# Kernel tuning notes

Measured on AMD Instinct MI355X. Metric: run time of the kernel, lower is better.

Reference implementation:

```python
import math
import jax, jax.numpy as jnp
import numpy as np

HEAD = 8
D_HEAD = 32
D_MODEL = 256
N = 20000
E_LOCAL = 80000
E_BOND = 60000
E_GLOBAL = 400000
MAX_DEG = 32
MAX_DIST = 64


def segment_softmax(x, seg, num_segments):
    # softmax over entries sharing the same segment id (scatter_softmax)
    m = jax.ops.segment_max(x, seg, num_segments=num_segments)
    e = jnp.exp(x - m[seg])
    s = jax.ops.segment_sum(e, seg, num_segments=num_segments)
    return e / s[seg]


def setup_inputs() -> dict:
    key = jax.random.key(0)
    ks = jax.random.split(key, 16)
    s_in = 1.0 / math.sqrt(D_MODEL)
    s_out = 1.0 / math.sqrt(2 * D_MODEL)
    dist_emb = jax.random.normal(ks[7], (MAX_DIST + 1, D_MODEL), jnp.float32) * 0.02
    dist_emb = dist_emb.at[MAX_DIST].set(0.0)  # padding_idx
    return {
        "f_node": jax.random.normal(ks[0], (N, D_MODEL), jnp.float32),
        "f_bond": jax.random.normal(ks[1], (E_BOND, D_MODEL), jnp.float32),
        "deg_matrix": jax.random.randint(ks[2], (N,), 0, MAX_DEG + 1),
        "dist_matrix": jax.random.randint(ks[3], (E_GLOBAL,), 0, MAX_DIST + 1),
        "bond_idx": jax.random.randint(ks[4], (2, E_LOCAL), 0, N),
        "query_idx": jax.random.randint(ks[5], (E_GLOBAL,), 0, N),
        "key_idx": jax.random.randint(ks[6], (E_GLOBAL,), 0, N),
        "attention_bond_idx": jnp.arange(E_BOND),
        "deg_emb": jax.random.normal(ks[8], (MAX_DEG + 1, D_MODEL), jnp.float32) * 0.02,
        "dist_emb": dist_emb,
        "Wq_w": jax.random.normal(ks[9], (D_MODEL, 2 * D_MODEL), jnp.float32) * s_in,
        "Wq_b": jnp.zeros((2 * D_MODEL,), jnp.float32),
        "Wk_w": jax.random.normal(ks[10], (D_MODEL, 2 * D_MODEL), jnp.float32) * s_in,
        "Wk_b": jnp.zeros((2 * D_MODEL,), jnp.float32),
        "Wv_w": jax.random.normal(ks[11], (D_MODEL, 2 * D_MODEL), jnp.float32) * s_in,
        "Wv_b": jnp.zeros((2 * D_MODEL,), jnp.float32),
        "out_w": jax.random.normal(ks[12], (2 * D_MODEL, D_MODEL), jnp.float32) * s_out,
        "out_b": jnp.zeros((D_MODEL,), jnp.float32),
        "bond_emb_w": jax.random.normal(ks[13], (D_MODEL, 2 * D_MODEL), jnp.float32) * s_in,
        "bond_emb_b": jnp.zeros((2 * D_MODEL,), jnp.float32),
        "bond_update_w": jax.random.normal(ks[14], (2 * D_MODEL, D_MODEL), jnp.float32) * s_out,
        "bond_update_b": jnp.zeros((D_MODEL,), jnp.float32),
    }


def reference(f_node, f_bond, deg_matrix, dist_matrix, bond_idx, query_idx, key_idx,
              attention_bond_idx, deg_emb, dist_emb, Wq_w, Wq_b, Wk_w, Wk_b, Wv_w, Wv_b,
              out_w, out_b, bond_emb_w, bond_emb_b, bond_update_w, bond_update_b):
    scale = 1.0 / math.sqrt(D_HEAD)
    n = f_node.shape[0]
    e_bond = f_bond.shape[0]

    f_deg = deg_emb[deg_matrix].reshape(n, HEAD, D_HEAD)                  # [N,H,Dh]
    ab_vb = f_bond @ bond_emb_w + bond_emb_b                               # [Eb,2D]
    attention_bond, value_bond = jnp.split(ab_vb, 2, axis=-1)
    attention_bond = attention_bond.reshape(e_bond, HEAD, D_HEAD)
    value_bond = value_bond.reshape(e_bond, HEAD, D_HEAD)
    f_dist = dist_emb[dist_matrix].reshape(-1, HEAD, D_HEAD)               # [Eg,H,Dh]

    q = (f_node @ Wq_w + Wq_b).reshape(n, 2 * HEAD, D_HEAD)
    k = (f_node @ Wk_w + Wk_b).reshape(n, 2 * HEAD, D_HEAD)
    v = (f_node @ Wv_w + Wv_b).reshape(n, 2 * HEAD, D_HEAD)
    q_local, q_global = q[:, :HEAD], q[:, HEAD:]
    k_local, k_global = k[:, :HEAD], k[:, HEAD:]
    v_local, v_global = v[:, :HEAD], v[:, HEAD:]

    src, dst = bond_idx[0], bond_idx[1]
    # ---- local (bond) attention ----
    score_local = q_local[dst] * k_local[src]                              # [El,H,Dh]
    score_local = score_local.at[:e_bond].add(attention_bond)
    score_local = score_local.sum(-1) * scale                              # [El,H]
    score_local = segment_softmax(score_local, dst, n)
    local_out = v_local[src].at[:e_bond].add(value_bond)
    local_out = local_out * score_local[:, :, None]
    local_out = jax.ops.segment_sum(local_out, dst, num_segments=n)
    local_out = local_out.reshape(n, HEAD * D_HEAD)

    # ---- global (distance) attention ----
    kg = k_global + f_deg
    score_global = q_global[query_idx] * kg[key_idx]                       # [Eg,H,Dh]
    score_global = score_global.at[attention_bond_idx].add(attention_bond)
    score_global = (score_global + f_dist).sum(-1) * scale                 # [Eg,H]
    score_global = segment_softmax(score_global, query_idx, n)
    global_out = v_global[key_idx] * score_global[:, :, None]
    global_out = jax.ops.segment_sum(global_out, query_idx, num_segments=n)
    global_out = global_out.reshape(n, HEAD * D_HEAD)

    out = jnp.concatenate([local_out, global_out], axis=-1) @ out_w + out_b  # [N,D]
    bond_out = jnp.concatenate([f_bond, out[src[:e_bond]]], axis=-1)
    bond_out = bond_out @ bond_update_w + bond_update_b                      # [Eb,D]
    return out, bond_out
```

## Files before the change

### kernel.cpp

```cpp
#include <hip/hip_runtime.h>
#include <math.h>

typedef unsigned short u16;
typedef unsigned int u32;
typedef __attribute__((ext_vector_type(8))) short s16x8;
typedef __attribute__((ext_vector_type(4))) unsigned short u16x4;
typedef __attribute__((ext_vector_type(4))) float f32x4;

__device__ __forceinline__ float bf2f(u16 x) { return __uint_as_float(((u32)x) << 16); }
__device__ __forceinline__ u16 f2bf(float f) {
    u32 u = __float_as_uint(f);
    u32 r = u + 0x7fffu + ((u >> 16) & 1u);
    return (u16)(r >> 16);
}

__device__ __forceinline__ void gll16(const u16* g, u16* l) {
    __builtin_amdgcn_global_load_lds((const __attribute__((address_space(1))) void*)g,
                                     (__attribute__((address_space(3))) void*)l,
                                     16, 0, 0);
}

template <int MODE>
__global__ __launch_bounds__(256) void gemm128(
    const u16* __restrict__ Abf, const u16* __restrict__ A2b,
    const u16* __restrict__ BT, const float* __restrict__ bias,
    u16* __restrict__ Cb, float* __restrict__ Cf, u16* __restrict__ C2b,
    const float* __restrict__ auxemb, const int* __restrict__ auxidx,
    float* __restrict__ absum, int M, int N, int K)
{
    __shared__ u16 lsmem[3 * 8192];

    const int tid = threadIdx.x;
    const int wave = tid >> 6;
    const int lane = tid & 63;
    const int l15 = lane & 15;
    const int quad = lane >> 4;
    const int wr = wave >> 1, wc = wave & 1;
    const int tileRow = blockIdx.y * 128;
    const int tileCol = blockIdx.x * 128;

    const int srow = tid >> 2;
    const int sk8 = (((tid & 3) ^ ((tid >> 3) & 3)) * 8);
    const int r0 = tileRow + srow, r1 = r0 + 64;

    const u16 *gA0, *gA1, *gA0b = nullptr, *gA1b = nullptr;
    if (MODE == 3) {
        gA0 = Abf + (size_t)r0 * 256 + sk8;
        gA1 = Abf + (size_t)r1 * 256 + sk8;
        gA0b = A2b + (size_t)auxidx[min(r0, M - 1)] * 256 + sk8;
        gA1b = A2b + (size_t)auxidx[min(r1, M - 1)] * 256 + sk8;
    } else {
        gA0 = Abf + (size_t)r0 * K + sk8;
        gA1 = Abf + (size_t)r1 * K + sk8;
    }
    const u16* gB0 = BT + (size_t)(tileCol + srow) * K + sk8;
    const u16* gB1 = BT + (size_t)(tileCol + 64 + srow) * K + sk8;

    const int lofs = tid * 8;

#define STAGE(TK, BI)                                                          \
    {                                                                          \
        u16* lbs = lsmem + (BI) * 8192;                                        \
        const int kk_ = (TK) * 32;                                             \
        if (MODE == 3) {                                                       \
            const u16* a0 = (kk_ < 256) ? gA0 + kk_ : gA0b + (kk_ - 256);      \
            const u16* a1 = (kk_ < 256) ? gA1 + kk_ : gA1b + (kk_ - 256);      \
            gll16(a0, lbs + lofs);                                             \
            gll16(a1, lbs + 2048 + lofs);                                      \
        } else {                                                               \
            gll16(gA0 + kk_, lbs + lofs);                                      \
            gll16(gA1 + kk_, lbs + 2048 + lofs);                               \
        }                                                                      \
        gll16(gB0 + kk_, lbs + 4096 + lofs);                                   \
        gll16(gB1 + kk_, lbs + 4096 + 2048 + lofs);                            \
    }

    f32x4 acc[4][4] = {};
    const int nt = K >> 5;

    STAGE(0, 0);
    if (nt > 1) STAGE(1, 1);

    const int xq8 = (quad ^ ((l15 >> 1) & 3)) * 8;
    const int aoff = (wr * 64 + l15) * 32 + xq8;
    const int boff = 4096 + (wc * 64 + l15) * 32 + xq8;

    int bc = 0;
    for (int t = 0; t < nt; ++t) {
        if (t + 1 < nt) asm volatile("s_waitcnt vmcnt(4)" ::: "memory");
        else            asm volatile("s_waitcnt vmcnt(0)" ::: "memory");
        __builtin_amdgcn_s_barrier();
        if (t + 2 < nt) {
            const int bs = (bc >= 1) ? bc - 1 : 2;
            STAGE(t + 2, bs);
        }

        const u16* lb = lsmem + bc * 8192;
        s16x8 a[4], b[4];
#pragma unroll
        for (int mi = 0; mi < 4; mi++)
            a[mi] = *(const s16x8*)(lb + aoff + mi * 512);
#pragma unroll
        for (int ni = 0; ni < 4; ni++)
            b[ni] = *(const s16x8*)(lb + boff + ni * 512);
#pragma unroll
        for (int mi = 0; mi < 4; mi++)
#pragma unroll
            for (int ni = 0; ni < 4; ni++)
                acc[mi][ni] = __builtin_amdgcn_mfma_f32_16x16x32_bf16(a[mi], b[ni],
                                                                      acc[mi][ni], 0, 0, 0);
        bc = (bc == 2) ? 0 : bc + 1;
    }
#undef STAGE

#pragma unroll
    for (int mi = 0; mi < 4; mi++) {
#pragma unroll
        for (int i = 0; i < 4; i++) {
            const int r = tileRow + wr * 64 + mi * 16 + quad * 4 + i;
            const bool rok = (r < M);
#pragma unroll
            for (int ni = 0; ni < 4; ni++) {
                const int c = tileCol + wc * 64 + ni * 16 + l15;
                float v = acc[mi][ni][i] + bias[c];
                if (MODE == 2) {
                    if (tileCol < 256) {
                        float s = v;
                        s += __shfl_xor(s, 1, 16);
                        s += __shfl_xor(s, 2, 16);
                        s += __shfl_xor(s, 4, 16);
                        s += __shfl_xor(s, 8, 16);
                        if (rok && l15 == 0) atomicAdd(&absum[r * 8 + (c >> 5)], s);
                    } else {
                        if (rok) Cb[(size_t)r * 256 + (c - 256)] = f2bf(v);
                    }
                } else if (MODE == 3) {
                    if (rok) Cf[(size_t)r * N + c] = v;
                } else if (MODE == 4) {
                    if (rok) {
                        Cf[(size_t)r * N + c] = v;
                        C2b[(size_t)r * N + c] = f2bf(v);
                    }
                } else {
                    const int which = c >> 9;
                    const int cc = c & 511;
                    if (which == 1 && cc >= 256)
                        v += auxemb[(size_t)auxidx[min(r, M - 1)] * 256 + (cc - 256)];
                    if (rok) Cb[((size_t)which * M + r) * 512 + cc] = f2bf(v);
                }
            }
        }
    }
}

__global__ __launch_bounds__(256) void cvt_pad(const float* __restrict__ A,
                                               u16* __restrict__ B, int M, int Mpad, int K)
{
    int t = blockIdx.x * 256 + threadIdx.x;
    if (t >= (Mpad * K) / 4) return;
    int r = (t * 4) / K;
    f32x4 v = {0.f, 0.f, 0.f, 0.f};
    if (r < M) v = *(const f32x4*)(A + (size_t)t * 4);
    u16x4 o;
#pragma unroll
    for (int j = 0; j < 4; j++) o[j] = f2bf(v[j]);
    *(u16x4*)(B + (size_t)t * 4) = o;
}

__global__ __launch_bounds__(256) void transpose_w(const float* __restrict__ B,
                                                   u16* __restrict__ BT, int K, int N)
{
    int t = blockIdx.x * 256 + threadIdx.x;
    if (t >= K * N) return;
    int n = t / K, k = t - n * K;
    BT[t] = f2bf(B[(size_t)k * N + n]);
}

__global__ __launch_bounds__(256) void concat_bias(const float* __restrict__ a,
                                                   const float* __restrict__ b,
                                                   const float* __restrict__ c,
                                                   float* __restrict__ o)
{
    int t = blockIdx.x * 256 + threadIdx.x;
    if (t < 512) o[t] = a[t];
    else if (t < 1024) o[t] = b[t - 512];
    else if (t < 1536) o[t] = c[t - 1024];
}

__global__ __launch_bounds__(256) void rowsum32f(const float* __restrict__ E,
                                                 float* __restrict__ S, int count)
{
    int t = blockIdx.x * 256 + threadIdx.x;
    if (t >= count) return;
    const float* p = E + (size_t)t * 32;
    float s = 0.f;
#pragma unroll
    for (int j = 0; j < 32; j++) s += p[j];
    S[t] = s;
}

__global__ __launch_bounds__(256) void hist_k(const int* __restrict__ idx,
                                              int* __restrict__ cnt, int E)
{
    int e = blockIdx.x * 256 + threadIdx.x;
    if (e < E) atomicAdd(&cnt[idx[e]], 1);
}

__global__ __launch_bounds__(1024) void scan_k(const int* __restrict__ cnt,
                                               int* __restrict__ offs,
                                               int* __restrict__ cursor, int n)
{
    __shared__ int part[1024];
    const int tid = threadIdx.x;
    const int per = (n + 1023) / 1024;
    int local[32];
    int s = 0;
    for (int j = 0; j < per; j++) {
        int idx = tid * per + j;
        int c = (idx < n) ? cnt[idx] : 0;
        local[j] = s;
        s += c;
    }
    part[tid] = s;
    __syncthreads();
    for (int st = 1; st < 1024; st <<= 1) {
        int v = (tid >= st) ? part[tid - st] : 0;
        __syncthreads();
        part[tid] += v;
        __syncthreads();
    }
    int pre = (tid == 0) ? 0 : part[tid - 1];
    for (int j = 0; j < per; j++) {
        int idx = tid * per + j;
        if (idx < n) { int o = pre + local[j]; offs[idx] = o; cursor[idx] = o; }
    }
    if (tid == 1023) offs[n] = part[1023];
}

__global__ __launch_bounds__(256) void scatter_k(const int* __restrict__ idx,
                                                 int* __restrict__ cursor,
                                                 int* __restrict__ list, int E)
{
    int e = blockIdx.x * 256 + threadIdx.x;
    if (e >= E) return;
    int pos = atomicAdd(&cursor[idx[e]], 1);
    list[pos] = e;
}

template <bool GLOB>
__device__ __forceinline__ void attn_half(
    const u16* __restrict__ qb, const u16* __restrict__ kb,
    const u16* __restrict__ vbuf, const u16* __restrict__ vb,
    const int* __restrict__ offs, const int* __restrict__ lst,
    const int* __restrict__ oth, const int* __restrict__ dist,
    const float* __restrict__ absum, const float* __restrict__ distsum,
    u16* __restrict__ out, int node, int EB, float scale)
{
    const int lane = threadIdx.x & 63;
    const int head = lane >> 3;
    const int cbase = (GLOB ? 256 : 0) + lane * 4;

    const u16x4 qv = *(const u16x4*)(qb + (size_t)node * 512 + cbase);
    const float q0 = bf2f(qv[0]), q1 = bf2f(qv[1]), q2 = bf2f(qv[2]), q3 = bf2f(qv[3]);

    const int s0 = offs[node], s1 = offs[node + 1];
    float a0 = 0.f, a1 = 0.f, a2 = 0.f, a3 = 0.f, den = 0.f;
    const u16x4 zv = {0, 0, 0, 0};

#define LOADS(S, IDX)                                                          \
    {                                                                          \
        e##S = __shfl(e_l, (IDX));                                             \
        const int src = __shfl(src_l, (IDX));                                  \
        kv##S = *(const u16x4*)(kb + (size_t)src * 512 + cbase);               \
        vv##S = *(const u16x4*)(vbuf + (size_t)src * 512 + cbase);             \
        ab##S = (e##S < EB) ? absum[e##S * 8 + head] : 0.f;                    \
        if (GLOB) {                                                            \
            const int d = __shfl(d_l, (IDX));                                  \
            ds##S = distsum[d * 8 + head];                                     \
        }                                                                      \
        if (!GLOB)                                                             \
            wv##S = (e##S < EB) ? *(const u16x4*)(vb + (size_t)e##S * 256 +    \
                                                  lane * 4)                    \
                                : zv;                                          \
    }

#define COMP(S)                                                                \
    {                                                                          \
        float t = q0 * bf2f(kv##S[0]) + q1 * bf2f(kv##S[1]) +                  \
                  q2 * bf2f(kv##S[2]) + q3 * bf2f(kv##S[3]);                   \
        t += __shfl_xor(t, 1);                                                 \
        t += __shfl_xor(t, 2);                                                 \
        t += __shfl_xor(t, 4);                                                 \
        t += ab##S;                                                            \
        if (GLOB) t += ds##S;                                                  \
        const float p = __expf(t * scale);                                     \
        den += p;                                                              \
        float v0 = bf2f(vv##S[0]), v1 = bf2f(vv##S[1]);                        \
        float v2 = bf2f(vv##S[2]), v3 = bf2f(vv##S[3]);                        \
        if (!GLOB) {                                                           \
            v0 += bf2f(wv##S[0]); v1 += bf2f(wv##S[1]);                        \
            v2 += bf2f(wv##S[2]); v3 += bf2f(wv##S[3]);                        \
        }                                                                      \
        a0 += p * v0; a1 += p * v1; a2 += p * v2; a3 += p * v3;                \
    }

    for (int base = s0; base < s1; base += 64) {
        const int cnt = min(64, s1 - base);
        const int gi = base + lane;
        int e_l = 0, src_l = 0, d_l = 0;
        if (gi < s1) {
            e_l = lst[gi];
            src_l = oth[e_l];
            if (GLOB) d_l = dist[e_l];
        }

        int eX, eY;
        u16x4 kvX, vvX, wvX = zv, kvY, vvY, wvY = zv;
        float abX, dsX = 0.f, abY, dsY = 0.f;

        LOADS(X, 0);
        int i = 0;
        for (; i + 2 <= cnt; i += 2) {
            LOADS(Y, i + 1);
            COMP(X);
            if (i + 2 < cnt) LOADS(X, i + 2);
            COMP(Y);
        }
        if (i < cnt) COMP(X);
    }
#undef LOADS
#undef COMP

    const float inv = (den > 0.f) ? 1.f / den : 0.f;
    u16x4 o;
    o[0] = f2bf(a0 * inv); o[1] = f2bf(a1 * inv);
    o[2] = f2bf(a2 * inv); o[3] = f2bf(a3 * inv);
    *(u16x4*)(out + (size_t)node * 512 + cbase) = o;
}

__global__ __launch_bounds__(256) void attn_fused(
    const u16* __restrict__ qb, const u16* __restrict__ kb,
    const u16* __restrict__ vbuf, const u16* __restrict__ vb,
    const int* __restrict__ offs_l, const int* __restrict__ list_l,
    const int* __restrict__ bsrc,
    const int* __restrict__ offs_g, const int* __restrict__ list_g,
    const int* __restrict__ kidx,
    const int* __restrict__ dist, const float* __restrict__ absum,
    const float* __restrict__ distsum, u16* __restrict__ out,
    int Nn, int EB, float scale)
{
    const int w = blockIdx.x * 4 + (threadIdx.x >> 6);
    if (w >= 2 * Nn) return;
    if (w < Nn)
        attn_half<false>(qb, kb, vbuf, vb, offs_l, list_l, bsrc, dist, absum,
                         distsum, out, w, EB, scale);
    else
        attn_half<true>(qb, kb, vbuf, vb, offs_g, list_g, kidx, dist, absum,
                        distsum, out, w - Nn, EB, scale);
}

extern "C" void kernel_launch(void* const* d_in, const int* in_sizes, int n_in,
                              void* d_out, int out_size, void* d_ws, size_t ws_size,
                              hipStream_t stream)
{
    const float* f_node  = (const float*)d_in[0];
    const float* f_bond  = (const float*)d_in[1];
    const int* deg       = (const int*)d_in[2];
    const int* dist      = (const int*)d_in[3];
    const int* bond_idx  = (const int*)d_in[4];
    const int* qidx      = (const int*)d_in[5];
    const int* kidx      = (const int*)d_in[6];
    const float* deg_emb = (const float*)d_in[8];
    const float* dist_emb= (const float*)d_in[9];
    const float* Wq_w = (const float*)d_in[10]; const float* Wq_b = (const float*)d_in[11];
    const float* Wk_w = (const float*)d_in[12]; const float* Wk_b = (const float*)d_in[13];
    const float* Wv_w = (const float*)d_in[14]; const float* Wv_b = (const float*)d_in[15];
    const float* out_w = (const float*)d_in[16]; const float* out_b = (const float*)d_in[17];
    const float* be_w  = (const float*)d_in[18]; const float* be_b  = (const float*)d_in[19];
    const float* bu_w  = (const float*)d_in[20]; const float* bu_b  = (const float*)d_in[21];

    const int N_ = in_sizes[0] / 256;
    const int EB = in_sizes[1] / 256;
    const int EL = in_sizes[4] / 2;
    const int EG = in_sizes[5];
    const float scale = 0.17677669529663689f;

    const int MPN = ((N_ + 127) / 128) * 128;
    const int MPB = ((EB + 127) / 128) * 128;

    const int* bsrc = bond_idx;
    const int* bdst = bond_idx + EL;

    u16* qb   = (u16*)d_ws;
    u16* kb   = qb + (size_t)N_ * 512;
    u16* vbuf = kb + (size_t)N_ * 512;
    u16* vb   = vbuf + (size_t)N_ * 512;
    u16* wT   = vb + (size_t)EB * 256;
    u16* wqT = wT;
    u16* wkT = wT + 131072;
    u16* wvT = wT + 2 * 131072;
    u16* beT = wT + 3 * 131072;
    u16* owT = wT + 4 * 131072;
    u16* buT = wT + 5 * 131072;
    float* distsum  = (float*)(wT + 6 * 131072);
    float* biasC    = distsum + 1024;
    u16* attn_out = (u16*)(biasC + 1536);
    u16* fnb      = attn_out;
    u16* fbb      = attn_out + (size_t)MPN * 512;
    u16* outb     = fbb + (size_t)MPB * 256;
    float* absum    = (float*)(outb + (size_t)N_ * 256);
    int*   cnt_l    = (int*)(absum + (size_t)EB * 8);
    int*   cnt_g    = cnt_l + N_;
    size_t zbytes   = ((size_t)EB * 8 + 2 * (size_t)N_) * 4;
    int*   offs_l   = cnt_g + N_;
    int*   offs_g   = offs_l + N_ + 4;
    int*   cur_l    = offs_g + N_ + 4;
    int*   cur_g    = cur_l + N_;
    int*   list_l   = cur_g + N_;
    int*   list_g   = list_l + EL;

    float* outp  = (float*)d_out;
    float* bondp = outp + (size_t)N_ * 256;

    hipMemsetAsync((void*)absum, 0, zbytes, stream);

    transpose_w<<<512, 256, 0, stream>>>(Wq_w, wqT, 256, 512);
    transpose_w<<<512, 256, 0, stream>>>(Wk_w, wkT, 256, 512);
    transpose_w<<<512, 256, 0, stream>>>(Wv_w, wvT, 256, 512);
    transpose_w<<<512, 256, 0, stream>>>(be_w, beT, 256, 512);
    transpose_w<<<512, 256, 0, stream>>>(out_w, owT, 512, 256);
    transpose_w<<<512, 256, 0, stream>>>(bu_w, buT, 512, 256);
    concat_bias<<<6, 256, 0, stream>>>(Wq_b, Wk_b, Wv_b, biasC);

    rowsum32f<<<3, 256, 0, stream>>>(dist_emb, distsum, 65 * 8);

    cvt_pad<<<(MPN * 256 / 4 + 255) / 256, 256, 0, stream>>>(f_node, fnb, N_, MPN, 256);
    cvt_pad<<<(MPB * 256 / 4 + 255) / 256, 256, 0, stream>>>(f_bond, fbb, EB, MPB, 256);

    hist_k<<<(EL + 255) / 256, 256, 0, stream>>>(bdst, cnt_l, EL);
    hist_k<<<(EG + 255) / 256, 256, 0, stream>>>(qidx, cnt_g, EG);
    scan_k<<<1, 1024, 0, stream>>>(cnt_l, offs_l, cur_l, N_);
    scan_k<<<1, 1024, 0, stream>>>(cnt_g, offs_g, cur_g, N_);
    scatter_k<<<(EL + 255) / 256, 256, 0, stream>>>(bdst, cur_l, list_l, EL);
    scatter_k<<<(EG + 255) / 256, 256, 0, stream>>>(qidx, cur_g, list_g, EG);

    dim3 g5(12, MPN / 128);
    gemm128<5><<<g5, 256, 0, stream>>>(fnb, nullptr, wqT, biasC, qb, nullptr, nullptr, deg_emb, deg, nullptr, N_, 1536, 256);

    dim3 gb(4, MPB / 128);
    gemm128<2><<<gb, 256, 0, stream>>>(fbb, nullptr, beT, be_b, vb, nullptr, nullptr, nullptr, nullptr, absum, EB, 512, 256);

    attn_fused<<<(2 * N_ + 3) / 4, 256, 0, stream>>>(qb, kb, vbuf, vb,
        offs_l, list_l, bsrc, offs_g, list_g, kidx, dist, absum, distsum,
        attn_out, N_, EB, scale);

    dim3 go(2, MPN / 128);
    gemm128<4><<<go, 256, 0, stream>>>(attn_out, nullptr, owT, out_b, nullptr, outp, outb, nullptr, nullptr, nullptr, N_, 256, 512);

    dim3 gu(2, MPB / 128);
    gemm128<3><<<gu, 256, 0, stream>>>(fbb, outb, buT, bu_b, nullptr, bondp, nullptr, nullptr, bsrc, nullptr, EB, 256, 512);
}
```

Baseline: 587.2 us.

## Restructure GEMM to BK=64 double-buffer with XCD remap; merge prep kernels

The GEMM kernel moves from a triple-buffered K=32 pipeline to a double-buffered K=64 tile with a new 8-way LDS swizzle. Workgroup IDs are remapped so neighbouring tiles land on the same XCD, to improve L2 reuse. The many small preprocessing launches (weight transposes, bias concat, dist rowsum, conversions, histogram, scan, scatter) are merged into a few combined kernels to cut launch overhead. Risks are less latency hiding from having fewer buffers and an extra barrier per iteration.

```diff
diff --git a/kernel.cpp b/kernel.cpp
--- a/kernel.cpp
+++ b/kernel.cpp
@@ -28,7 +28,7 @@
     const float* __restrict__ auxemb, const int* __restrict__ auxidx,
     float* __restrict__ absum, int M, int N, int K)
 {
-    __shared__ u16 lsmem[3 * 8192];
+    __shared__ u16 lsmem[2 * 16384];
 
     const int tid = threadIdx.x;
     const int wave = tid >> 6;
@@ -36,80 +36,84 @@
     const int l15 = lane & 15;
     const int quad = lane >> 4;
     const int wr = wave >> 1, wc = wave & 1;
-    const int tileRow = blockIdx.y * 128;
-    const int tileCol = blockIdx.x * 128;
-
-    const int srow = tid >> 2;
-    const int sk8 = (((tid & 3) ^ ((tid >> 3) & 3)) * 8);
-    const int r0 = tileRow + srow, r1 = r0 + 64;
-
-    const u16 *gA0, *gA1, *gA0b = nullptr, *gA1b = nullptr;
-    if (MODE == 3) {
-        gA0 = Abf + (size_t)r0 * 256 + sk8;
-        gA1 = Abf + (size_t)r1 * 256 + sk8;
-        gA0b = A2b + (size_t)auxidx[min(r0, M - 1)] * 256 + sk8;
-        gA1b = A2b + (size_t)auxidx[min(r1, M - 1)] * 256 + sk8;
-    } else {
-        gA0 = Abf + (size_t)r0 * K + sk8;
-        gA1 = Abf + (size_t)r1 * K + sk8;
-    }
-    const u16* gB0 = BT + (size_t)(tileCol + srow) * K + sk8;
-    const u16* gB1 = BT + (size_t)(tileCol + 64 + srow) * K + sk8;
-
-    const int lofs = tid * 8;
-
-#define STAGE(TK, BI)                                                          \
+
+    const int gx = gridDim.x;
+    const int nwg = gx * gridDim.y;
+    int flat = blockIdx.y * gx + blockIdx.x;
+    {
+        const int q = nwg >> 3, r8 = nwg & 7;
+        const int xcd = flat & 7, loc = flat >> 3;
+        flat = (xcd < r8 ? xcd * (q + 1) : r8 * (q + 1) + (xcd - r8) * q) + loc;
+    }
+    const int tileRow = (flat / gx) * 128;
+    const int tileCol = (flat % gx) * 128;
+
+    const int srow = tid >> 3;
+    const int ks = ((tid & 7) ^ (srow & 7)) * 8;
+
+    const u16 *gA[4], *gB[4], *gA2[4];
+#pragma unroll
+    for (int j = 0; j < 4; j++) {
+        const int ra = j * 32 + srow;
+        const int pa = (MODE == 3) ? 256 : K;
+        gA[j] = Abf + (size_t)(tileRow + ra) * pa + ks;
+        gB[j] = BT + (size_t)(tileCol + ra) * K + ks;
+        if (MODE == 3)
+            gA2[j] = A2b + (size_t)auxidx[min(tileRow + ra, M - 1)] * 256 + ks;
+        else
+            gA2[j] = nullptr;
+    }
+
+#define STAGE(TK, BUF)                                                         \
     {                                                                          \
-        u16* lbs = lsmem + (BI) * 8192;                                        \
-        const int kk_ = (TK) * 32;                                             \
-        if (MODE == 3) {                                                       \
-            const u16* a0 = (kk_ < 256) ? gA0 + kk_ : gA0b + (kk_ - 256);      \
-            const u16* a1 = (kk_ < 256) ? gA1 + kk_ : gA1b + (kk_ - 256);      \
-            gll16(a0, lbs + lofs);                                             \
-            gll16(a1, lbs + 2048 + lofs);                                      \
-        } else {                                                               \
-            gll16(gA0 + kk_, lbs + lofs);                                      \
-            gll16(gA1 + kk_, lbs + 2048 + lofs);                               \
+        u16* lb_ = lsmem + (BUF)*16384;                                        \
+        const int kk_ = (TK)*64;                                               \
+        _Pragma("unroll")                                                      \
+        for (int j = 0; j < 4; j++) {                                          \
+            const u16* sa;                                                     \
+            if (MODE == 3) sa = (kk_ < 256) ? gA[j] + kk_ : gA2[j] + (kk_ - 256); \
+            else sa = gA[j] + kk_;                                             \
+            gll16(sa, lb_ + j * 2048 + tid * 8);                               \
+            gll16(gB[j] + kk_, lb_ + 8192 + j * 2048 + tid * 8);               \
         }                                                                      \
-        gll16(gB0 + kk_, lbs + 4096 + lofs);                                   \
-        gll16(gB1 + kk_, lbs + 4096 + 2048 + lofs);                            \
     }
 
     f32x4 acc[4][4] = {};
-    const int nt = K >> 5;
+    const int nt = K >> 6;
 
     STAGE(0, 0);
-    if (nt > 1) STAGE(1, 1);
-
-    const int xq8 = (quad ^ ((l15 >> 1) & 3)) * 8;
-    const int aoff = (wr * 64 + l15) * 32 + xq8;
-    const int boff = 4096 + (wc * 64 + l15) * 32 + xq8;
-
-    int bc = 0;
+    STAGE(1, 1);
+
     for (int t = 0; t < nt; ++t) {
-        if (t + 1 < nt) asm volatile("s_waitcnt vmcnt(4)" ::: "memory");
+        if (t + 2 < nt) asm volatile("s_waitcnt vmcnt(8)" ::: "memory");
         else            asm volatile("s_waitcnt vmcnt(0)" ::: "memory");
         __builtin_amdgcn_s_barrier();
-        if (t + 2 < nt) {
-            const int bs = (bc >= 1) ? bc - 1 : 2;
-            STAGE(t + 2, bs);
-        }
-
-        const u16* lb = lsmem + bc * 8192;
-        s16x8 a[4], b[4];
-#pragma unroll
-        for (int mi = 0; mi < 4; mi++)
-            a[mi] = *(const s16x8*)(lb + aoff + mi * 512);
-#pragma unroll
-        for (int ni = 0; ni < 4; ni++)
-            b[ni] = *(const s16x8*)(lb + boff + ni * 512);
-#pragma unroll
-        for (int mi = 0; mi < 4; mi++)
+        __builtin_amdgcn_sched_barrier(0);
+
+        const u16* lb = lsmem + (t & 1) * 16384;
+#pragma unroll
+        for (int kh = 0; kh < 2; kh++) {
+            const int xk = ((quad + 4 * kh) ^ (l15 & 7)) * 8;
+            s16x8 a[4], b[4];
+#pragma unroll
+            for (int mi = 0; mi < 4; mi++)
+                a[mi] = *(const s16x8*)(lb + (wr * 64 + mi * 16 + l15) * 64 + xk);
 #pragma unroll
             for (int ni = 0; ni < 4; ni++)
-                acc[mi][ni] = __builtin_amdgcn_mfma_f32_16x16x32_bf16(a[mi], b[ni],
-                                                                      acc[mi][ni], 0, 0, 0);
-        bc = (bc == 2) ? 0 : bc + 1;
+                b[ni] = *(const s16x8*)(lb + 8192 + (wc * 64 + ni * 16 + l15) * 64 + xk);
+#pragma unroll
+            for (int mi = 0; mi < 4; mi++)
+#pragma unroll
+                for (int ni = 0; ni < 4; ni++)
+                    acc[mi][ni] = __builtin_amdgcn_mfma_f32_16x16x32_bf16(
+                        a[mi], b[ni], acc[mi][ni], 0, 0, 0);
+        }
+
+        __builtin_amdgcn_sched_barrier(0);
+        asm volatile("s_waitcnt lgkmcnt(0)" ::: "memory");
+        __builtin_amdgcn_s_barrier();
+        __builtin_amdgcn_sched_barrier(0);
+        if (t + 2 < nt) STAGE(t + 2, t & 1);
     }
 #undef STAGE
 
@@ -153,63 +157,91 @@
     }
 }
 
-__global__ __launch_bounds__(256) void cvt_pad(const float* __restrict__ A,
-                                               u16* __restrict__ B, int M, int Mpad, int K)
-{
-    int t = blockIdx.x * 256 + threadIdx.x;
-    if (t >= (Mpad * K) / 4) return;
-    int r = (t * 4) / K;
-    f32x4 v = {0.f, 0.f, 0.f, 0.f};
-    if (r < M) v = *(const f32x4*)(A + (size_t)t * 4);
-    u16x4 o;
-#pragma unroll
-    for (int j = 0; j < 4; j++) o[j] = f2bf(v[j]);
-    *(u16x4*)(B + (size_t)t * 4) = o;
-}
-
-__global__ __launch_bounds__(256) void transpose_w(const float* __restrict__ B,
-                                                   u16* __restrict__ BT, int K, int N)
-{
-    int t = blockIdx.x * 256 + threadIdx.x;
-    if (t >= K * N) return;
-    int n = t / K, k = t - n * K;
-    BT[t] = f2bf(B[(size_t)k * N + n]);
-}
-
-__global__ __launch_bounds__(256) void concat_bias(const float* __restrict__ a,
-                                                   const float* __restrict__ b,
-                                                   const float* __restrict__ c,
-                                                   float* __restrict__ o)
-{
-    int t = blockIdx.x * 256 + threadIdx.x;
-    if (t < 512) o[t] = a[t];
-    else if (t < 1024) o[t] = b[t - 512];
-    else if (t < 1536) o[t] = c[t - 1024];
-}
-
-__global__ __launch_bounds__(256) void rowsum32f(const float* __restrict__ E,
-                                                 float* __restrict__ S, int count)
-{
-    int t = blockIdx.x * 256 + threadIdx.x;
-    if (t >= count) return;
-    const float* p = E + (size_t)t * 32;
-    float s = 0.f;
-#pragma unroll
-    for (int j = 0; j < 32; j++) s += p[j];
-    S[t] = s;
-}
-
-__global__ __launch_bounds__(256) void hist_k(const int* __restrict__ idx,
-                                              int* __restrict__ cnt, int E)
-{
-    int e = blockIdx.x * 256 + threadIdx.x;
-    if (e < E) atomicAdd(&cnt[idx[e]], 1);
-}
-
-__global__ __launch_bounds__(1024) void scan_k(const int* __restrict__ cnt,
-                                               int* __restrict__ offs,
-                                               int* __restrict__ cursor, int n)
-{
+__global__ __launch_bounds__(256) void prep_k(
+    const float* __restrict__ Wq_w, const float* __restrict__ Wk_w,
+    const float* __restrict__ Wv_w, const float* __restrict__ be_w,
+    const float* __restrict__ out_w, const float* __restrict__ bu_w,
+    u16* __restrict__ wT,
+    const float* __restrict__ Wq_b, const float* __restrict__ Wk_b,
+    const float* __restrict__ Wv_b, float* __restrict__ biasC,
+    const float* __restrict__ dist_emb, float* __restrict__ distsum)
+{
+    const int b = blockIdx.x;
+    if (b < 3072) {
+        const int idx6 = b >> 9;
+        const int r = ((b & 511) << 8) + threadIdx.x;
+        const float* s = (idx6 == 0) ? Wq_w : (idx6 == 1) ? Wk_w
+                       : (idx6 == 2) ? Wv_w : (idx6 == 3) ? be_w
+                       : (idx6 == 4) ? out_w : bu_w;
+        u16* dst = wT + (size_t)idx6 * 131072;
+        if (idx6 < 4) {
+            const int n = r >> 8, k = r & 255;
+            dst[r] = f2bf(s[(size_t)k * 512 + n]);
+        } else {
+            const int n = r >> 9, k = r & 511;
+            dst[r] = f2bf(s[(size_t)k * 256 + n]);
+        }
+    } else {
+        const int u = (b - 3072) * 256 + threadIdx.x;
+        if (u < 512) biasC[u] = Wq_b[u];
+        else if (u < 1024) biasC[u] = Wk_b[u - 512];
+        else if (u < 1536) biasC[u] = Wv_b[u - 1024];
+        else if (u < 1536 + 520) {
+            const float* p = dist_emb + (size_t)(u - 1536) * 32;
+            float sm = 0.f;
+#pragma unroll
+            for (int j = 0; j < 32; j++) sm += p[j];
+            distsum[u - 1536] = sm;
+        }
+    }
+}
+
+__global__ __launch_bounds__(256) void cvt2_k(
+    const float* __restrict__ f_node, const float* __restrict__ f_bond,
+    u16* __restrict__ fnb, u16* __restrict__ fbb,
+    int N_, int MPN, int EB, int MPB)
+{
+    const int t = blockIdx.x * 256 + threadIdx.x;
+    const int q1 = MPN * 64;
+    const int q2 = MPB * 64;
+    if (t < q1) {
+        const int r = t >> 6;
+        f32x4 v = {0.f, 0.f, 0.f, 0.f};
+        if (r < N_) v = *(const f32x4*)(f_node + (size_t)t * 4);
+        u16x4 o;
+#pragma unroll
+        for (int j = 0; j < 4; j++) o[j] = f2bf(v[j]);
+        *(u16x4*)(fnb + (size_t)t * 4) = o;
+    } else if (t < q1 + q2) {
+        const int u = t - q1;
+        const int r = u >> 6;
+        f32x4 v = {0.f, 0.f, 0.f, 0.f};
+        if (r < EB) v = *(const f32x4*)(f_bond + (size_t)u * 4);
+        u16x4 o;
+#pragma unroll
+        for (int j = 0; j < 4; j++) o[j] = f2bf(v[j]);
+        *(u16x4*)(fbb + (size_t)u * 4) = o;
+    }
+}
+
+__global__ __launch_bounds__(256) void hist2_k(const int* __restrict__ bdst,
+                                               const int* __restrict__ qidx,
+                                               int* __restrict__ cnt,
+                                               int N_, int EL, int EG)
+{
+    const int e = blockIdx.x * 256 + threadIdx.x;
+    if (e < EL) atomicAdd(&cnt[bdst[e]], 1);
+    else if (e < EL + EG) atomicAdd(&cnt[N_ + qidx[e - EL]], 1);
+}
+
+__global__ __launch_bounds__(1024) void scan2_k(
+    const int* __restrict__ cnt_l, int* __restrict__ offs_l, int* __restrict__ cur_l,
+    const int* __restrict__ cnt_g, int* __restrict__ offs_g, int* __restrict__ cur_g,
+    int n)
+{
+    const int* cnt = blockIdx.x ? cnt_g : cnt_l;
+    int* offs = blockIdx.x ? offs_g : offs_l;
+    int* cursor = blockIdx.x ? cur_g : cur_l;
     __shared__ int part[1024];
     const int tid = threadIdx.x;
     const int per = (n + 1023) / 1024;
@@ -237,14 +269,20 @@
     if (tid == 1023) offs[n] = part[1023];
 }
 
-__global__ __launch_bounds__(256) void scatter_k(const int* __restrict__ idx,
-                                                 int* __restrict__ cursor,
-                                                 int* __restrict__ list, int E)
-{
-    int e = blockIdx.x * 256 + threadIdx.x;
-    if (e >= E) return;
-    int pos = atomicAdd(&cursor[idx[e]], 1);
-    list[pos] = e;
+__global__ __launch_bounds__(256) void scatter2_k(
+    const int* __restrict__ bdst, const int* __restrict__ qidx,
+    int* __restrict__ cur_l, int* __restrict__ cur_g,
+    int* __restrict__ list_l, int* __restrict__ list_g, int EL, int EG)
+{
+    const int e = blockIdx.x * 256 + threadIdx.x;
+    if (e < EL) {
+        int pos = atomicAdd(&cur_l[bdst[e]], 1);
+        list_l[pos] = e;
+    } else if (e < EL + EG) {
+        const int e2 = e - EL;
+        int pos = atomicAdd(&cur_g[qidx[e2]], 1);
+        list_g[pos] = e2;
+    }
 }
 
 template <bool GLOB>
@@ -397,8 +435,6 @@
     u16* vb   = vbuf + (size_t)N_ * 512;
     u16* wT   = vb + (size_t)EB * 256;
     u16* wqT = wT;
-    u16* wkT = wT + 131072;
-    u16* wvT = wT + 2 * 131072;
     u16* beT = wT + 3 * 131072;
     u16* owT = wT + 4 * 131072;
     u16* buT = wT + 5 * 131072;
@@ -424,25 +460,17 @@
 
     hipMemsetAsync((void*)absum, 0, zbytes, stream);
 
-    transpose_w<<<512, 256, 0, stream>>>(Wq_w, wqT, 256, 512);
-    transpose_w<<<512, 256, 0, stream>>>(Wk_w, wkT, 256, 512);
-    transpose_w<<<512, 256, 0, stream>>>(Wv_w, wvT, 256, 512);
-    transpose_w<<<512, 256, 0, stream>>>(be_w, beT, 256, 512);
-    transpose_w<<<512, 256, 0, stream>>>(out_w, owT, 512, 256);
-    transpose_w<<<512, 256, 0, stream>>>(bu_w, buT, 512, 256);
-    concat_bias<<<6, 256, 0, stream>>>(Wq_b, Wk_b, Wv_b, biasC);
-
-    rowsum32f<<<3, 256, 0, stream>>>(dist_emb, distsum, 65 * 8);
-
-    cvt_pad<<<(MPN * 256 / 4 + 255) / 256, 256, 0, stream>>>(f_node, fnb, N_, MPN, 256);
-    cvt_pad<<<(MPB * 256 / 4 + 255) / 256, 256, 0, stream>>>(f_bond, fbb, EB, MPB, 256);
-
-    hist_k<<<(EL + 255) / 256, 256, 0, stream>>>(bdst, cnt_l, EL);
-    hist_k<<<(EG + 255) / 256, 256, 0, stream>>>(qidx, cnt_g, EG);
-    scan_k<<<1, 1024, 0, stream>>>(cnt_l, offs_l, cur_l, N_);
-    scan_k<<<1, 1024, 0, stream>>>(cnt_g, offs_g, cur_g, N_);
-    scatter_k<<<(EL + 255) / 256, 256, 0, stream>>>(bdst, cur_l, list_l, EL);
-    scatter_k<<<(EG + 255) / 256, 256, 0, stream>>>(qidx, cur_g, list_g, EG);
+    prep_k<<<3072 + 9, 256, 0, stream>>>(Wq_w, Wk_w, Wv_w, be_w, out_w, bu_w,
+                                         wT, Wq_b, Wk_b, Wv_b, biasC,
+                                         dist_emb, distsum);
+
+    cvt2_k<<<(MPN * 64 + MPB * 64 + 255) / 256, 256, 0, stream>>>(
+        f_node, f_bond, fnb, fbb, N_, MPN, EB, MPB);
+
+    hist2_k<<<(EL + EG + 255) / 256, 256, 0, stream>>>(bdst, qidx, cnt_l, N_, EL, EG);
+    scan2_k<<<2, 1024, 0, stream>>>(cnt_l, offs_l, cur_l, cnt_g, offs_g, cur_g, N_);
+    scatter2_k<<<(EL + EG + 255) / 256, 256, 0, stream>>>(bdst, qidx, cur_l, cur_g,
+                                                          list_l, list_g, EL, EG);
 
     dim3 g5(12, MPN / 128);
     gemm128<5><<<g5, 256, 0, stream>>>(fnb, nullptr, wqT, biasC, qb, nullptr, nullptr, deg_emb, deg, nullptr, N_, 1536, 256);
```

Result: faster. 539.7 us (-8.1%).
